# Performance work log

Hardware: AMD Instinct MI355X
Metric: run time of the kernel (lower is better)

## Reference

```python
import jax, jax.numpy as jnp
import numpy as np

S, E, CAP = 4096, 64, 128


def setup_inputs() -> dict:
    key = jax.random.key(0)
    k1, k2 = jax.random.split(key)
    logits = jax.random.normal(k1, (S, E), dtype=jnp.float32)
    noise = jax.random.normal(k2, (S, E), dtype=jnp.float32)
    return {"logits": logits, "noise": noise, "capacity": CAP}


def reference(logits, noise, capacity):
    # logits, noise: [S, E]; capacity: python int
    gates = jax.nn.softmax(logits, axis=1)                      # [S, E]
    num_experts = gates.shape[1]

    # top-1 expert
    indices1_s = jnp.argmax(gates, axis=1)                      # [S]
    mask1 = jax.nn.one_hot(indices1_s, num_experts, dtype=jnp.int32)

    # top-2 expert from noised logits with top-1 masked out
    logits_w_noise = logits + noise
    neg_min = jnp.finfo(logits.dtype).min
    logits_except1 = jnp.where(mask1 > 0, neg_min, logits_w_noise)
    indices2_s = jnp.argmax(logits_except1, axis=1)
    mask2 = jax.nn.one_hot(indices2_s, num_experts, dtype=jnp.int32)

    # capacity locations (running count per expert over tokens)
    locations1 = jnp.cumsum(mask1, axis=0) - 1                  # [S, E]
    locations2 = jnp.cumsum(mask2, axis=0) - 1
    locations2 = locations2 + jnp.sum(mask1, axis=0, keepdims=True)

    # load-balancing aux loss
    me = jnp.mean(gates, axis=0)
    ce = jnp.mean(mask1.astype(logits.dtype), axis=0)
    l_aux = jnp.mean(me * ce) * num_experts * num_experts

    # drop tokens over capacity
    mask1 = mask1 * (locations1 < capacity).astype(mask1.dtype)
    mask2 = mask2 * (locations2 < capacity).astype(mask2.dtype)

    locations1_s = jnp.sum(locations1 * mask1, axis=1)          # [S]
    locations2_s = jnp.sum(locations2 * mask2, axis=1)

    mask1_f = mask1.astype(logits.dtype)
    mask2_f = mask2.astype(logits.dtype)
    gates1_s = jnp.einsum('se,se->s', gates, mask1_f)
    gates2_s = jnp.einsum('se,se->s', gates, mask2_f)
    denom_s = jnp.maximum(gates1_s + gates2_s, jnp.finfo(logits.dtype).eps)
    gates1_s = gates1_s / denom_s
    gates2_s = gates2_s / denom_s

    gates1 = gates1_s[:, None] * mask1_f                        # [S, E]
    gates2 = gates2_s[:, None] * mask2_f

    locations1_sc = jax.nn.one_hot(locations1_s, capacity, dtype=logits.dtype)
    locations2_sc = jax.nn.one_hot(locations2_s, capacity, dtype=logits.dtype)

    combine_weights = (gates1[:, :, None] * locations1_sc[:, None, :]
                       + gates2[:, :, None] * locations2_sc[:, None, :])  # [S, E, C]
    dispatch_mask = combine_weights.astype(bool)
    return l_aux, combine_weights, dispatch_mask
```

## Files before the change

kernel.cpp:

```cpp
#include <hip/hip_runtime.h>
#include <float.h>
#include <math.h>

#define SS 4096
#define EE 64
#define CAPC 128
#define ROW 8192
#define SEC (4096LL * 64 * 128)
#define NBLK 256
#define TPB_TOK 16

__global__ __launch_bounds__(1024) void k1_gate(
    const float* __restrict__ logits,
    const float* __restrict__ noise,
    int*   __restrict__ bc1,
    int*   __restrict__ bc2,
    float* __restrict__ pg,
    int*   __restrict__ tokmeta,
    float2* __restrict__ tokg)
{
    const int tid  = threadIdx.x;
    const int wave = tid >> 6;
    const int lane = tid & 63;
    const int b    = blockIdx.x;

    __shared__ int   s_idx1[TPB_TOK], s_idx2[TPB_TOK];
    __shared__ float s_gate[TPB_TOK][64];

    const int s = b * TPB_TOK + wave;
    const float l = logits[s * EE + lane];
    const float n = noise [s * EE + lane];

    float v = l; int bi = lane;
    #pragma unroll
    for (int off = 32; off; off >>= 1) {
        float v2 = __shfl_xor(v, off, 64);
        int   i2 = __shfl_xor(bi, off, 64);
        if (v2 > v || (v2 == v && i2 < bi)) { v = v2; bi = i2; }
    }
    const int idx1 = bi;

    float e = expf(l - v);
    float sum = e;
    #pragma unroll
    for (int off = 32; off; off >>= 1) sum += __shfl_xor(sum, off, 64);
    const float gate = e / sum;

    float lw = (lane == idx1) ? -FLT_MAX : (l + n);
    float v2v = lw; int bi2 = lane;
    #pragma unroll
    for (int off = 32; off; off >>= 1) {
        float q  = __shfl_xor(v2v, off, 64);
        int   i2 = __shfl_xor(bi2, off, 64);
        if (q > v2v || (q == v2v && i2 < bi2)) { v2v = q; bi2 = i2; }
    }
    const int idx2 = bi2;

    s_gate[wave][lane] = gate;
    const float g1v = __shfl(gate, idx1, 64);
    const float g2v = __shfl(gate, idx2, 64);
    if (lane == 0) {
        s_idx1[wave] = idx1;
        s_idx2[wave] = idx2;
        tokg[s] = make_float2(g1v, g2v);
    }
    __syncthreads();

    if (tid < 64) {
        int c1 = 0, c2 = 0;
        float gs = 0.f;
        #pragma unroll
        for (int j = 0; j < TPB_TOK; ++j) {
            c1 += (s_idx1[j] == tid);
            c2 += (s_idx2[j] == tid);
            gs += s_gate[j][tid];
        }
        bc1[b * 64 + tid] = c1;
        bc2[b * 64 + tid] = c2;
        pg [b * 64 + tid] = gs;
    } else if (tid < 64 + TPB_TOK) {
        const int t = tid - 64;
        const int m1 = s_idx1[t], m2 = s_idx2[t];
        int r1 = 0, r2 = 0;
        for (int j = 0; j < t; ++j) {
            r1 += (s_idx1[j] == m1);
            r2 += (s_idx2[j] == m2);
        }
        tokmeta[b * TPB_TOK + t] = m1 | (m2 << 6) | (r1 << 12) | (r2 << 17);
    }
}

__global__ __launch_bounds__(256) void k2_scan_scatter(
    const int*   __restrict__ bc1,
    const int*   __restrict__ bc2,
    const float* __restrict__ pg,
    const int*   __restrict__ tokmeta,
    const float2* __restrict__ tokg,
    float* __restrict__ out)
{
    const int tid = threadIdx.x;
    const int b   = blockIdx.x;

    __shared__ int   s_off1[64], s_off2[64], s_cnt1[64];
    __shared__ float s_gs[64];

    if (tid < 64) {
        int o1 = 0, mine = 0;
        #pragma unroll 8
        for (int blk = 0; blk < NBLK; ++blk) {
            if (blk == b) mine = o1;
            o1 += bc1[blk * 64 + tid];
        }
        s_off1[tid] = mine;
        s_cnt1[tid] = o1;
    } else if (tid < 128) {
        const int e = tid - 64;
        int o2 = 0, mine = 0;
        #pragma unroll 8
        for (int blk = 0; blk < NBLK; ++blk) {
            if (blk == b) mine = o2;
            o2 += bc2[blk * 64 + e];
        }
        s_off2[e] = mine;
    } else if (tid < 192 && b == 0) {
        const int e = tid - 128;
        float gs = 0.f;
        #pragma unroll 8
        for (int blk = 0; blk < NBLK; ++blk) gs += pg[blk * 64 + e];
        s_gs[e] = gs;
    }
    __syncthreads();

    if (tid < TPB_TOK) {
        const int s = b * TPB_TOK + tid;
        const int m = tokmeta[s];
        const int i1  =  m        & 63;
        const int i2  = (m >> 6)  & 63;
        const int lr1 = (m >> 12) & 31;
        const int lr2 = (m >> 17) & 31;
        const float2 g = tokg[s];
        const int loc1 = lr1 + s_off1[i1];
        const int loc2 = lr2 + s_off2[i2] + s_cnt1[i2];
        float g1 = g.x, g2 = g.y;
        const bool k1 = loc1 < CAPC, k2 = loc2 < CAPC;
        g1 = k1 ? g1 : 0.f;
        g2 = k2 ? g2 : 0.f;
        const float denom = fmaxf(g1 + g2, 1.1920929e-07f);
        g1 /= denom;
        g2 /= denom;
        float* combine = out + 1;
        float* mask    = out + 1 + SEC;
        const long base = (long)s * ROW;
        if (k1 && g1 != 0.f) {
            const long p = base + (long)i1 * CAPC + loc1;
            combine[p] = g1;
            mask[p]    = 1.f;
        }
        if (k2 && g2 != 0.f) {
            const long p = base + (long)i2 * CAPC + loc2;
            combine[p] = g2;
            mask[p]    = 1.f;
        }
    } else if (tid == 64 + TPB_TOK && b == 0) {
        float prod = 0.f;
        #pragma unroll 8
        for (int e = 0; e < 64; ++e) prod += s_gs[e] * (float)s_cnt1[e];
        out[0] = prod * (float)EE / ((float)SS * (float)SS);
    }
}

extern "C" void kernel_launch(void* const* d_in, const int* in_sizes, int n_in,
                              void* d_out, int out_size, void* d_ws, size_t ws_size,
                              hipStream_t stream) {
    const float* logits = (const float*)d_in[0];
    const float* noise  = (const float*)d_in[1];
    float* out = (float*)d_out;

    char* ws = (char*)d_ws;
    int*    bc1     = (int*)   (ws + 0);
    int*    bc2     = (int*)   (ws + 65536);
    float*  pg      = (float*) (ws + 131072);
    int*    tokmeta = (int*)   (ws + 196608);
    float2* tokg    = (float2*)(ws + 212992);

    k1_gate<<<NBLK, 1024, 0, stream>>>(logits, noise, bc1, bc2, pg,
                                       tokmeta, tokg);
    hipMemsetAsync(d_out, 0, (size_t)out_size * sizeof(float), stream);
    k2_scan_scatter<<<NBLK, 256, 0, stream>>>(bc1, bc2, pg, tokmeta, tokg, out);
}
```

Measured before the change: 280.8 us.

## Fuse output zero-fill into gating kernel and shrink gate blocks

Replaces the separate hipMemsetAsync of the large combine/dispatch output with extra blocks in the gating kernel that write zeros as float4 stores. The gate blocks now use 256 threads, with each wave handling four tokens in turn. This removes one stream operation and lets the zero-fill run alongside the gating work. The cost is that the fill's speed now depends on the hand-written store kernel rather than the runtime memset.

```diff
diff --git a/kernel.cpp b/kernel.cpp
--- a/kernel.cpp
+++ b/kernel.cpp
@@ -7,62 +7,79 @@
 #define CAPC 128
 #define ROW 8192
 #define SEC (4096LL * 64 * 128)
-#define NBLK 256
+#define NGATE 256
+#define NFILL 4096
 #define TPB_TOK 16
 
-__global__ __launch_bounds__(1024) void k1_gate(
+__global__ __launch_bounds__(256) void k1_gate_fill(
     const float* __restrict__ logits,
     const float* __restrict__ noise,
     int*   __restrict__ bc1,
     int*   __restrict__ bc2,
     float* __restrict__ pg,
     int*   __restrict__ tokmeta,
-    float2* __restrict__ tokg)
+    float2* __restrict__ tokg,
+    float* __restrict__ out)
 {
-    const int tid  = threadIdx.x;
+    const int tid = threadIdx.x;
+
+    if (blockIdx.x >= NGATE) {
+        const int fb = blockIdx.x - NGATE;
+        float4* p = (float4*)out + (long)fb * 4096;
+        const float4 z = make_float4(0.f, 0.f, 0.f, 0.f);
+        #pragma unroll
+        for (int i = 0; i < 16; ++i) p[i * 256 + tid] = z;
+        if (fb == NFILL - 1 && tid == 0) out[2 * SEC] = 0.f;
+        return;
+    }
+
+    const int b    = blockIdx.x;
     const int wave = tid >> 6;
     const int lane = tid & 63;
-    const int b    = blockIdx.x;
 
     __shared__ int   s_idx1[TPB_TOK], s_idx2[TPB_TOK];
     __shared__ float s_gate[TPB_TOK][64];
 
-    const int s = b * TPB_TOK + wave;
-    const float l = logits[s * EE + lane];
-    const float n = noise [s * EE + lane];
-
-    float v = l; int bi = lane;
     #pragma unroll
-    for (int off = 32; off; off >>= 1) {
-        float v2 = __shfl_xor(v, off, 64);
-        int   i2 = __shfl_xor(bi, off, 64);
-        if (v2 > v || (v2 == v && i2 < bi)) { v = v2; bi = i2; }
-    }
-    const int idx1 = bi;
-
-    float e = expf(l - v);
-    float sum = e;
-    #pragma unroll
-    for (int off = 32; off; off >>= 1) sum += __shfl_xor(sum, off, 64);
-    const float gate = e / sum;
-
-    float lw = (lane == idx1) ? -FLT_MAX : (l + n);
-    float v2v = lw; int bi2 = lane;
-    #pragma unroll
-    for (int off = 32; off; off >>= 1) {
-        float q  = __shfl_xor(v2v, off, 64);
-        int   i2 = __shfl_xor(bi2, off, 64);
-        if (q > v2v || (q == v2v && i2 < bi2)) { v2v = q; bi2 = i2; }
-    }
-    const int idx2 = bi2;
-
-    s_gate[wave][lane] = gate;
-    const float g1v = __shfl(gate, idx1, 64);
-    const float g2v = __shfl(gate, idx2, 64);
-    if (lane == 0) {
-        s_idx1[wave] = idx1;
-        s_idx2[wave] = idx2;
-        tokg[s] = make_float2(g1v, g2v);
+    for (int t4 = 0; t4 < 4; ++t4) {
+        const int t = wave * 4 + t4;
+        const int s = b * TPB_TOK + t;
+        const float l = logits[s * EE + lane];
+        const float n = noise [s * EE + lane];
+
+        float v = l; int bi = lane;
+        #pragma unroll
+        for (int off = 32; off; off >>= 1) {
+            float v2 = __shfl_xor(v, off, 64);
+            int   i2 = __shfl_xor(bi, off, 64);
+            if (v2 > v || (v2 == v && i2 < bi)) { v = v2; bi = i2; }
+        }
+        const int idx1 = bi;
+
+        float e = expf(l - v);
+        float sum = e;
+        #pragma unroll
+        for (int off = 32; off; off >>= 1) sum += __shfl_xor(sum, off, 64);
+        const float gate = e / sum;
+
+        float lw = (lane == idx1) ? -FLT_MAX : (l + n);
+        float v2v = lw; int bi2 = lane;
+        #pragma unroll
+        for (int off = 32; off; off >>= 1) {
+            float q  = __shfl_xor(v2v, off, 64);
+            int   i2 = __shfl_xor(bi2, off, 64);
+            if (q > v2v || (q == v2v && i2 < bi2)) { v2v = q; bi2 = i2; }
+        }
+        const int idx2 = bi2;
+
+        s_gate[t][lane] = gate;
+        const float g1v = __shfl(gate, idx1, 64);
+        const float g2v = __shfl(gate, idx2, 64);
+        if (lane == 0) {
+            s_idx1[t] = idx1;
+            s_idx2[t] = idx2;
+            tokg[s] = make_float2(g1v, g2v);
+        }
     }
     __syncthreads();
 
@@ -107,7 +124,7 @@
     if (tid < 64) {
         int o1 = 0, mine = 0;
         #pragma unroll 8
-        for (int blk = 0; blk < NBLK; ++blk) {
+        for (int blk = 0; blk < NGATE; ++blk) {
             if (blk == b) mine = o1;
             o1 += bc1[blk * 64 + tid];
         }
@@ -117,7 +134,7 @@
         const int e = tid - 64;
         int o2 = 0, mine = 0;
         #pragma unroll 8
-        for (int blk = 0; blk < NBLK; ++blk) {
+        for (int blk = 0; blk < NGATE; ++blk) {
             if (blk == b) mine = o2;
             o2 += bc2[blk * 64 + e];
         }
@@ -126,7 +143,7 @@
         const int e = tid - 128;
         float gs = 0.f;
         #pragma unroll 8
-        for (int blk = 0; blk < NBLK; ++blk) gs += pg[blk * 64 + e];
+        for (int blk = 0; blk < NGATE; ++blk) gs += pg[blk * 64 + e];
         s_gs[e] = gs;
     }
     __syncthreads();
@@ -183,8 +200,7 @@
     int*    tokmeta = (int*)   (ws + 196608);
     float2* tokg    = (float2*)(ws + 212992);
 
-    k1_gate<<<NBLK, 1024, 0, stream>>>(logits, noise, bc1, bc2, pg,
-                                       tokmeta, tokg);
-    hipMemsetAsync(d_out, 0, (size_t)out_size * sizeof(float), stream);
-    k2_scan_scatter<<<NBLK, 256, 0, stream>>>(bc1, bc2, pg, tokmeta, tokg, out);
+    k1_gate_fill<<<NGATE + NFILL, 256, 0, stream>>>(logits, noise, bc1, bc2, pg,
+                                                    tokmeta, tokg, out);
+    k2_scan_scatter<<<NGATE, 256, 0, stream>>>(bc1, bc2, pg, tokmeta, tokg, out);
 }
```

Result: faster. 274.3 us, median of 2 (-2.3%).
